# Performance work log

Hardware: AMD Instinct MI355X
Metric: run time of the kernel (lower is better)

The kernel has to match this reference:

```python
import jax, jax.numpy as jnp
import numpy as np

N = 100000          # total nodes
F = 128             # in_features
B = 1000            # number of graphs
NPG = 100           # nodes per graph (contiguous)
DEG = 16            # avg degree
E = B * NPG * DEG   # total edges (intra-graph)
K_RATIO = 0.8
KNUM = max(1, int(K_RATIO * NPG))  # nodes kept per graph = 80


def setup_inputs() -> dict:
    key = jax.random.key(0)
    k1, k2, k3, k4 = jax.random.split(key, 4)
    x = jax.random.normal(k1, (N, F), dtype=jnp.float32)
    # intra-graph random edges: offset each block of NPG*DEG edges by its graph's base node id
    offs = (jnp.arange(E, dtype=jnp.int32) // (NPG * DEG)) * NPG
    src = jax.random.randint(k2, (E,), 0, NPG, dtype=jnp.int32) + offs
    dst = jax.random.randint(k3, (E,), 0, NPG, dtype=jnp.int32) + offs
    edge_index = jnp.stack([src, dst], axis=0)
    batch = (jnp.arange(N, dtype=jnp.int32) // NPG).astype(jnp.int32)
    limit = float(np.sqrt(6.0 / (F + 1)))  # xavier_uniform for (F,1)
    theta_att = jax.random.uniform(k4, (F, 1), dtype=jnp.float32, minval=-limit, maxval=limit)
    return {"x": x, "edge_index": edge_index, "batch": batch, "theta_att": theta_att}


def reference(x, edge_index, batch, theta_att):
    num_nodes = x.shape[0]
    # add self loops with weight 1
    loops = jnp.arange(num_nodes, dtype=edge_index.dtype)
    row = jnp.concatenate([edge_index[0], loops])
    col = jnp.concatenate([edge_index[1], loops])
    w = jnp.ones(row.shape[0], dtype=x.dtype)
    # symmetric degree normalization (degree counted over row, as in torch code)
    deg = jax.ops.segment_sum(w, row, num_segments=num_nodes)
    dis = jnp.where(deg > 0, jax.lax.rsqrt(deg), jnp.zeros((), x.dtype))
    norm = dis[row] * w * dis[col]
    # scatter-add: agg[dst] += x[src] * norm
    agg = jax.ops.segment_sum(x[row] * norm[:, None], col, num_segments=num_nodes)
    z = (agg @ theta_att)[:, 0]                     # (N,)
    # per-graph top-k: graphs are contiguous and equal-sized -> reshape
    zb = z.reshape(B, NPG)
    _, pos = jax.lax.top_k(zb, KNUM)                # (B, KNUM) positions within each graph
    pos = jnp.sort(pos, axis=1)                     # global sort of keep_idx == per-graph sort here
    keep = (pos + jnp.arange(B, dtype=pos.dtype)[:, None] * NPG).reshape(-1)  # (B*KNUM,)
    scale = jax.nn.sigmoid(z[keep])[:, None]
    x_new = x[keep] * scale                         # (B*KNUM, F)
    batch_new = batch[keep]
    # subgraph with relabeled nodes; dropped edges padded with -1 (fixed shape for jit)
    node_mask = jnp.zeros(num_nodes, dtype=bool).at[keep].set(True)
    new_id = jnp.cumsum(node_mask.astype(jnp.int32)) - 1
    emask = node_mask[edge_index[0]] & node_mask[edge_index[1]]
    edge_index_new = jnp.where(emask[None, :], new_id[edge_index], -1)
    return x_new, edge_index_new, batch_new
```

## Files before the change

### kernel.cpp

```cpp
#include <hip/hip_runtime.h>


#define NPG   100
#define EPG   1600
#define KNUM  80
#define FDIM  128

__global__ __launch_bounds__(256)
void sagpool_fused2(const float* __restrict__ x,
                    const int*   __restrict__ ei,
                    const float* __restrict__ theta,
                    float* __restrict__ out,
                    int E_total, int out_x_elems)
{
    const int g    = blockIdx.x;
    const int tid  = threadIdx.x;
    const int wave = tid >> 6;
    const int lane = tid & 63;
    const int base = g * NPG;

    __shared__ int4   sh_edge4[EPG / 4];
    __shared__ float4 sh_theta4[FDIM / 4];
    __shared__ int    sh_deg[NPG];
    __shared__ double sh_s[NPG];
    __shared__ double sh_dis[NPG];
    __shared__ double sh_a[NPG];
    __shared__ double sh_zp[4][NPG];
    __shared__ double sh_z[NPG];
    __shared__ unsigned long long sh_mask[2];
    __shared__ int    sh_newid[NPG];
    __shared__ int    sh_keepnode[KNUM];
    __shared__ float  sh_scale[KNUM];

    int* sh_edge = (int*)sh_edge4;

    if (tid < NPG)      sh_deg[tid] = 1;
    if (tid < FDIM / 4) sh_theta4[tid] = ((const float4*)theta)[tid];
    for (int i = tid; i < 4 * NPG; i += 256) ((double*)sh_zp)[i] = 0.0;
    __syncthreads();

    if (tid < 128) {
        if (tid < NPG) {
            const float4* xr = (const float4*)(x + (size_t)(base + tid) * FDIM);
            double acc = 0.0;
            #pragma unroll
            for (int k = 0; k < FDIM / 4; ++k) {
                float4 xv = xr[k];
                float4 th = sh_theta4[k];
                acc += (double)xv.x * th.x + (double)xv.y * th.y
                     + (double)xv.z * th.z + (double)xv.w * th.w;
            }
            sh_s[tid] = acc;
        }
    } else {
        const int t2 = tid - 128;
        const int4* src4 = (const int4*)(ei + (size_t)g * EPG);
        const int4* dst4 = (const int4*)(ei + (size_t)E_total + (size_t)g * EPG);
        for (int slot = t2; slot < EPG / 4; slot += 128) {
            int4 s4 = src4[slot];
            int4 d4 = dst4[slot];
            s4.x -= base; s4.y -= base; s4.z -= base; s4.w -= base;
            d4.x -= base; d4.y -= base; d4.z -= base; d4.w -= base;
            int4 p;
            p.x = s4.x | (d4.x << 16);
            p.y = s4.y | (d4.y << 16);
            p.z = s4.z | (d4.z << 16);
            p.w = s4.w | (d4.w << 16);
            sh_edge4[slot] = p;
            atomicAdd(&sh_deg[s4.x], 1);
            atomicAdd(&sh_deg[s4.y], 1);
            atomicAdd(&sh_deg[s4.z], 1);
            atomicAdd(&sh_deg[s4.w], 1);
        }
    }
    __syncthreads();

    if (tid < NPG) {
        double dis = 1.0 / sqrt((double)sh_deg[tid]);
        sh_dis[tid] = dis;
        sh_a[tid]   = sh_s[tid] * dis;
    }
    __syncthreads();

    {
        double* zp = sh_zp[wave];
        for (int j = tid; j < EPG; j += 256) {
            int p = sh_edge[j];
            int s = p & 0xffff;
            int d = p >> 16;
            atomicAdd(&zp[d], sh_a[s] * sh_dis[d]);
        }
    }
    __syncthreads();

    double zi = 0.0;
    if (tid < NPG) {
        zi = sh_a[tid] * sh_dis[tid]
           + sh_zp[0][tid] + sh_zp[1][tid] + sh_zp[2][tid] + sh_zp[3][tid];
        sh_z[tid] = zi;
    }
    __syncthreads();

    bool kept = false;
    if (tid < NPG) {
        int rank = 0;
        for (int j = 0; j < NPG; ++j) {
            double zj = sh_z[j];
            rank += (int)((zj > zi) | ((zj == zi) & (j < tid)));
        }
        kept = rank < KNUM;
        sh_newid[tid] = -1;
    }
    unsigned long long m = __ballot(kept);
    if (lane == 0 && wave < 2) sh_mask[wave] = m;
    __syncthreads();

    if (kept) {
        int before = (wave == 0)
            ? __popcll(sh_mask[0] & ((1ull << lane) - 1ull))
            : __popcll(sh_mask[0]) + __popcll(sh_mask[1] & ((1ull << lane) - 1ull));
        int row = g * KNUM + before;
        sh_newid[tid]       = row;
        sh_keepnode[before] = tid;
        sh_scale[before]    = (float)(1.0 / (1.0 + exp(-zi)));
        out[(size_t)out_x_elems + 2 * (size_t)E_total + row] = (float)g;
    }
    __syncthreads();

    for (int idx = tid; idx < KNUM * FDIM / 4; idx += 256) {
        int   row  = idx >> 5;
        int   c    = idx & 31;
        int   node = sh_keepnode[row];
        float sc   = sh_scale[row];
        float4 xv  = ((const float4*)(x + (size_t)(base + node) * FDIM))[c];
        float4 o;
        o.x = xv.x * sc; o.y = xv.y * sc; o.z = xv.z * sc; o.w = xv.w * sc;
        ((float4*)(out + (size_t)(g * KNUM + row) * FDIM))[c] = o;
    }

    float* e0 = out + out_x_elems;
    float* e1 = e0 + E_total;
    for (int slot = tid; slot < EPG / 4; slot += 256) {
        int4 p = sh_edge4[slot];
        float4 o0, o1;
        {
            int s = p.x & 0xffff, d = p.x >> 16;
            int a = sh_newid[s], b = sh_newid[d];
            bool v = (a >= 0) && (b >= 0);
            o0.x = v ? (float)a : -1.0f; o1.x = v ? (float)b : -1.0f;
        }
        {
            int s = p.y & 0xffff, d = p.y >> 16;
            int a = sh_newid[s], b = sh_newid[d];
            bool v = (a >= 0) && (b >= 0);
            o0.y = v ? (float)a : -1.0f; o1.y = v ? (float)b : -1.0f;
        }
        {
            int s = p.z & 0xffff, d = p.z >> 16;
            int a = sh_newid[s], b = sh_newid[d];
            bool v = (a >= 0) && (b >= 0);
            o0.z = v ? (float)a : -1.0f; o1.z = v ? (float)b : -1.0f;
        }
        {
            int s = p.w & 0xffff, d = p.w >> 16;
            int a = sh_newid[s], b = sh_newid[d];
            bool v = (a >= 0) && (b >= 0);
            o0.w = v ? (float)a : -1.0f; o1.w = v ? (float)b : -1.0f;
        }
        ((float4*)e0)[(size_t)g * (EPG / 4) + slot] = o0;
        ((float4*)e1)[(size_t)g * (EPG / 4) + slot] = o1;
    }
}

extern "C" void kernel_launch(void* const* d_in, const int* in_sizes, int n_in,
                              void* d_out, int out_size, void* d_ws, size_t ws_size,
                              hipStream_t stream)
{
    const float* x     = (const float*)d_in[0];
    const int*   ei    = (const int*)d_in[1];
    const float* theta = (const float*)d_in[3];
    float* out = (float*)d_out;

    const int N = in_sizes[0] / FDIM;
    const int E = in_sizes[1] / 2;
    const int B = N / NPG;
    const int out_x_elems = B * KNUM * FDIM;

    sagpool_fused2<<<dim3(B), dim3(256), 0, stream>>>(x, ei, theta, out, E, out_x_elems);
}
```

Baseline: 121.1 us.

## Coalesce x and edge loads across all threads with shuffle-reduced dot products

Each block now has all 256 threads issue their global loads up front: edges in one or two int4 slots per thread, and the graph's whole x tile spread across 13 float4 registers per thread. Per-node dot products with theta are then reduced across 32 lanes with xor shuffles, replacing the old scheme where 100 threads each walked a 512-byte row serially. This gives coalesced, high-parallelism memory traffic and lets the edge and x fetches overlap. The cost is higher register pressure, which may lower occupancy, plus extra shuffle work done in double precision.

After: 115.7 us. -4.4%, faster.

```diff
diff --git a/kernel.cpp b/kernel.cpp
--- a/kernel.cpp
+++ b/kernel.cpp
@@ -5,9 +5,11 @@
 #define EPG   1600
 #define KNUM  80
 #define FDIM  128
+#define NF4   (NPG * FDIM / 4)
+#define NE4   (EPG / 4)
 
 __global__ __launch_bounds__(256)
-void sagpool_fused2(const float* __restrict__ x,
+void sagpool_fused3(const float* __restrict__ x,
                     const int*   __restrict__ ei,
                     const float* __restrict__ theta,
                     float* __restrict__ out,
@@ -19,8 +21,7 @@
     const int lane = tid & 63;
     const int base = g * NPG;
 
-    __shared__ int4   sh_edge4[EPG / 4];
-    __shared__ float4 sh_theta4[FDIM / 4];
+    __shared__ int4   sh_edge4[NE4];
     __shared__ int    sh_deg[NPG];
     __shared__ double sh_s[NPG];
     __shared__ double sh_dis[NPG];
@@ -34,44 +35,63 @@
 
     int* sh_edge = (int*)sh_edge4;
 
-    if (tid < NPG)      sh_deg[tid] = 1;
-    if (tid < FDIM / 4) sh_theta4[tid] = ((const float4*)theta)[tid];
+    const float4 th = ((const float4*)theta)[lane & 31];
+
+    if (tid < NPG) sh_deg[tid] = 1;
     for (int i = tid; i < 4 * NPG; i += 256) ((double*)sh_zp)[i] = 0.0;
     __syncthreads();
 
+    const int4* src4 = (const int4*)(ei + (size_t)g * EPG);
+    const int4* dst4 = (const int4*)(ei + (size_t)E_total + (size_t)g * EPG);
+    const bool  hasE1 = tid < (NE4 - 256);
+    int4 es0 = src4[tid];
+    int4 ed0 = dst4[tid];
+    int4 es1, ed1;
+    if (hasE1) { es1 = src4[256 + tid]; ed1 = dst4[256 + tid]; }
+
+    const float4* xb4 = (const float4*)(x + (size_t)base * FDIM);
+    float4 v[12];
+    #pragma unroll
+    for (int i = 0; i < 12; ++i) v[i] = xb4[i * 256 + tid];
+    const bool has13 = tid < (NF4 - 12 * 256);
+    float4 v12;
+    if (has13) v12 = xb4[12 * 256 + tid];
+
+    {
+        int4 s4 = es0, d4 = ed0;
+        s4.x -= base; s4.y -= base; s4.z -= base; s4.w -= base;
+        d4.x -= base; d4.y -= base; d4.z -= base; d4.w -= base;
+        int4 p; p.x = s4.x | (d4.x << 16); p.y = s4.y | (d4.y << 16);
+                p.z = s4.z | (d4.z << 16); p.w = s4.w | (d4.w << 16);
+        sh_edge4[tid] = p;
+        atomicAdd(&sh_deg[s4.x], 1); atomicAdd(&sh_deg[s4.y], 1);
+        atomicAdd(&sh_deg[s4.z], 1); atomicAdd(&sh_deg[s4.w], 1);
+    }
+    if (hasE1) {
+        int4 s4 = es1, d4 = ed1;
+        s4.x -= base; s4.y -= base; s4.z -= base; s4.w -= base;
+        d4.x -= base; d4.y -= base; d4.z -= base; d4.w -= base;
+        int4 p; p.x = s4.x | (d4.x << 16); p.y = s4.y | (d4.y << 16);
+                p.z = s4.z | (d4.z << 16); p.w = s4.w | (d4.w << 16);
+        sh_edge4[256 + tid] = p;
+        atomicAdd(&sh_deg[s4.x], 1); atomicAdd(&sh_deg[s4.y], 1);
+        atomicAdd(&sh_deg[s4.z], 1); atomicAdd(&sh_deg[s4.w], 1);
+    }
+
+    #pragma unroll
+    for (int i = 0; i < 12; ++i) {
+        double p = (double)v[i].x * th.x + (double)v[i].y * th.y
+                 + (double)v[i].z * th.z + (double)v[i].w * th.w;
+        #pragma unroll
+        for (int m = 1; m <= 16; m <<= 1) p += __shfl_xor(p, m, 64);
+        if ((lane & 31) == 0) sh_s[(i * 256 + tid) >> 5] = p;
+    }
     if (tid < 128) {
-        if (tid < NPG) {
-            const float4* xr = (const float4*)(x + (size_t)(base + tid) * FDIM);
-            double acc = 0.0;
-            #pragma unroll
-            for (int k = 0; k < FDIM / 4; ++k) {
-                float4 xv = xr[k];
-                float4 th = sh_theta4[k];
-                acc += (double)xv.x * th.x + (double)xv.y * th.y
-                     + (double)xv.z * th.z + (double)xv.w * th.w;
-            }
-            sh_s[tid] = acc;
-        }
-    } else {
-        const int t2 = tid - 128;
-        const int4* src4 = (const int4*)(ei + (size_t)g * EPG);
-        const int4* dst4 = (const int4*)(ei + (size_t)E_total + (size_t)g * EPG);
-        for (int slot = t2; slot < EPG / 4; slot += 128) {
-            int4 s4 = src4[slot];
-            int4 d4 = dst4[slot];
-            s4.x -= base; s4.y -= base; s4.z -= base; s4.w -= base;
-            d4.x -= base; d4.y -= base; d4.z -= base; d4.w -= base;
-            int4 p;
-            p.x = s4.x | (d4.x << 16);
-            p.y = s4.y | (d4.y << 16);
-            p.z = s4.z | (d4.z << 16);
-            p.w = s4.w | (d4.w << 16);
-            sh_edge4[slot] = p;
-            atomicAdd(&sh_deg[s4.x], 1);
-            atomicAdd(&sh_deg[s4.y], 1);
-            atomicAdd(&sh_deg[s4.z], 1);
-            atomicAdd(&sh_deg[s4.w], 1);
-        }
+        double p = (double)v12.x * th.x + (double)v12.y * th.y
+                 + (double)v12.z * th.z + (double)v12.w * th.w;
+        #pragma unroll
+        for (int m = 1; m <= 16; m <<= 1) p += __shfl_xor(p, m, 64);
+        if ((lane & 31) == 0) sh_s[(12 * 256 + tid) >> 5] = p;
     }
     __syncthreads();
 
@@ -140,35 +160,35 @@
 
     float* e0 = out + out_x_elems;
     float* e1 = e0 + E_total;
-    for (int slot = tid; slot < EPG / 4; slot += 256) {
+    for (int slot = tid; slot < NE4; slot += 256) {
         int4 p = sh_edge4[slot];
         float4 o0, o1;
         {
             int s = p.x & 0xffff, d = p.x >> 16;
             int a = sh_newid[s], b = sh_newid[d];
-            bool v = (a >= 0) && (b >= 0);
-            o0.x = v ? (float)a : -1.0f; o1.x = v ? (float)b : -1.0f;
+            bool vv = (a >= 0) && (b >= 0);
+            o0.x = vv ? (float)a : -1.0f; o1.x = vv ? (float)b : -1.0f;
         }
         {
             int s = p.y & 0xffff, d = p.y >> 16;
             int a = sh_newid[s], b = sh_newid[d];
-            bool v = (a >= 0) && (b >= 0);
-            o0.y = v ? (float)a : -1.0f; o1.y = v ? (float)b : -1.0f;
+            bool vv = (a >= 0) && (b >= 0);
+            o0.y = vv ? (float)a : -1.0f; o1.y = vv ? (float)b : -1.0f;
         }
         {
             int s = p.z & 0xffff, d = p.z >> 16;
             int a = sh_newid[s], b = sh_newid[d];
-            bool v = (a >= 0) && (b >= 0);
-            o0.z = v ? (float)a : -1.0f; o1.z = v ? (float)b : -1.0f;
+            bool vv = (a >= 0) && (b >= 0);
+            o0.z = vv ? (float)a : -1.0f; o1.z = vv ? (float)b : -1.0f;
         }
         {
             int s = p.w & 0xffff, d = p.w >> 16;
             int a = sh_newid[s], b = sh_newid[d];
-            bool v = (a >= 0) && (b >= 0);
-            o0.w = v ? (float)a : -1.0f; o1.w = v ? (float)b : -1.0f;
-        }
-        ((float4*)e0)[(size_t)g * (EPG / 4) + slot] = o0;
-        ((float4*)e1)[(size_t)g * (EPG / 4) + slot] = o1;
+            bool vv = (a >= 0) && (b >= 0);
+            o0.w = vv ? (float)a : -1.0f; o1.w = vv ? (float)b : -1.0f;
+        }
+        ((float4*)e0)[(size_t)g * NE4 + slot] = o0;
+        ((float4*)e1)[(size_t)g * NE4 + slot] = o1;
     }
 }
 
@@ -186,5 +206,5 @@
     const int B = N / NPG;
     const int out_x_elems = B * KNUM * FDIM;
 
-    sagpool_fused2<<<dim3(B), dim3(256), 0, stream>>>(x, ei, theta, out, E, out_x_elems);
+    sagpool_fused3<<<dim3(B), dim3(256), 0, stream>>>(x, ei, theta, out, E, out_x_elems);
 }
```
